# Kernel optimization log

Hardware: AMD Instinct MI355X
Metric: run time of the kernel (lower is better)

Reference implementation:

```python
import jax, jax.numpy as jnp
import numpy as np


def layer_norm(x, gamma, beta, eps=1e-6):
    # Torch module uses unbiased std (ddof=1) and divides by (std + eps)
    mean = x.mean(-1, keepdims=True)
    std = jnp.std(x, axis=-1, keepdims=True, ddof=1)
    return gamma * (x - mean) / (std + eps) + beta


def gelu_erf(x):
    return 0.5 * x * (1.0 + jax.lax.erf(x / jnp.sqrt(jnp.asarray(2.0, x.dtype))))


def setup_inputs() -> dict:
    B, S, D, H, F = 32, 512, 1024, 16, 4096
    key = jax.random.key(0)
    ks = jax.random.split(key, 16)
    w = lambda k, shp: (jax.random.normal(k, shp, jnp.float32) * 0.02)
    return {
        "x": jax.random.normal(ks[0], (B, S, D), jnp.float32),
        "mask": jax.random.randint(ks[1], (B, S), 0, 2).astype(jnp.int32),
        "adj": jax.random.normal(ks[2], (B, 1, S, S), jnp.float32) * 0.1,
        "num_head": H,
        "Wq": w(ks[3], (D, D)), "bq": jnp.zeros((D,), jnp.float32),
        "Wk": w(ks[4], (D, D)), "bk": jnp.zeros((D,), jnp.float32),
        "Wv": w(ks[5], (D, D)), "bv": jnp.zeros((D,), jnp.float32),
        "Wo": w(ks[6], (D, D)), "bo": jnp.zeros((D,), jnp.float32),
        "W1": w(ks[7], (D, F)), "b1": jnp.zeros((F,), jnp.float32),
        "W2": w(ks[8], (F, D)), "b2": jnp.zeros((D,), jnp.float32),
        "gamma": jnp.ones((D,), jnp.float32),
        "beta": jnp.zeros((D,), jnp.float32),
    }


def reference(x, mask, adj, num_head, Wq, bq, Wk, bk, Wv, bv, Wo, bo,
              W1, b1, W2, b2, gamma, beta):
    B, S, D = x.shape
    H = num_head
    dk = D // H
    split = lambda t: t.reshape(B, S, H, dk).transpose(0, 2, 1, 3)  # [B,H,S,dk]
    q = split(x @ Wq + bq)
    k = split(x @ Wk + bk)
    v = split(x @ Wv + bv)
    scores = jnp.einsum('bhqd,bhkd->bhqk', q, k) / np.float32(np.sqrt(dk))
    m = mask[:, None, None, :].astype(x.dtype)  # [B,1,1,S]
    scores = scores + m * jnp.asarray(-1e9, x.dtype) + adj
    attn = jax.nn.softmax(scores, axis=-1)
    ctx = jnp.einsum('bhqk,bhkd->bhqd', attn, v)
    ctx = ctx.transpose(0, 2, 1, 3).reshape(B, S, D)
    attn_out = ctx @ Wo + bo  # dropout is identity at eval
    out1 = layer_norm(x + attn_out, gamma, beta)
    ffn = gelu_erf(out1 @ W1 + b1) @ W2 + b2
    return layer_norm(out1 + ffn, gamma, beta)
```

## Files before the change

### kernel.cpp

```cpp
#include <hip/hip_runtime.h>
#include <stdint.h>
#include <math.h>

typedef unsigned short u16;
typedef __attribute__((ext_vector_type(8))) __bf16 bf16x8;
typedef __attribute__((ext_vector_type(4))) float f32x4;
typedef __attribute__((ext_vector_type(4))) unsigned short u16x4;

__device__ __forceinline__ float b2f(u16 u) {
    unsigned int i = ((unsigned int)u) << 16;
    float f; __builtin_memcpy(&f, &i, 4); return f;
}
__device__ __forceinline__ u16 f2b(float f) {
    unsigned int i; __builtin_memcpy(&i, &f, 4);
    i = (i + 0x7FFFu + ((i >> 16) & 1u)) >> 16;
    return (u16)i;
}
__device__ __forceinline__ bf16x8 ld8_cvt(const float* p) {
    float4 f0 = *(const float4*)p, f1 = *(const float4*)(p + 4);
    u16 t[8] = {f2b(f0.x), f2b(f0.y), f2b(f0.z), f2b(f0.w),
                f2b(f1.x), f2b(f1.y), f2b(f1.z), f2b(f1.w)};
    bf16x8 r; __builtin_memcpy(&r, t, 16); return r;
}

__device__ __forceinline__ void glds16(const u16* g, u16* l) {
    __builtin_amdgcn_global_load_lds(
        (const __attribute__((address_space(1))) void*)g,
        (__attribute__((address_space(3))) void*)l, 16, 0, 0);
}

__global__ __launch_bounds__(256) void transpose_f32_bf16(
    const float* __restrict__ in, u16* __restrict__ out, int R, int C)
{
    __shared__ float t[32][33];
    int bx = blockIdx.x * 32, by = blockIdx.y * 32;
    int x = threadIdx.x, y = threadIdx.y;
    #pragma unroll
    for (int j = 0; j < 32; j += 8)
        t[y + j][x] = in[(size_t)(by + y + j) * C + bx + x];
    __syncthreads();
    #pragma unroll
    for (int j = 0; j < 32; j += 8)
        out[(size_t)(bx + y + j) * R + by + x] = f2b(t[x][y + j]);
}

__global__ __launch_bounds__(256) void cvt_f32_bf16(
    const float* __restrict__ in, u16* __restrict__ out)
{
    size_t i = ((size_t)blockIdx.x * 256 + threadIdx.x) * 8;
    *(bf16x8*)(out + i) = ld8_cvt(in + i);
}

template<int EPI, int BN>
__global__ __launch_bounds__(256) void gemm_bt(
    const u16* __restrict__ A, const u16* __restrict__ Bt, int N, int K,
    u16* __restrict__ C, const float* __restrict__ bias,
    u16* __restrict__ qo, u16* __restrict__ ko, u16* __restrict__ vo,
    const float* __restrict__ bq, const float* __restrict__ bk,
    const float* __restrict__ bv)
{
    __shared__ __align__(16) u16 Asm[128 * 32];
    __shared__ __align__(16) u16 Bsm[BN * 32];
    const int tid  = threadIdx.x;
    const int lane = tid & 63;
    const int wave = tid >> 6;
    const int lrow = lane & 15, quad = lane >> 4;
    const int bm = blockIdx.x * 128, bn = blockIdx.y * BN;

    const int srow = tid >> 2;
    const int skol = (tid & 3) * 8;
    const u16* gA0 = A  + (size_t)(bm + srow) * K + skol;
    const u16* gA1 = gA0 + (size_t)64 * K;
    const u16* gB0 = Bt + (size_t)(bn + srow) * K + skol;
    const u16* gB1 = gB0 + (size_t)64 * K;

    const int wm = wave >> 1, wn = wave & 1;
    const int NT = (BN == 128) ? 4 : 2;
    f32x4 acc[4][(BN == 128) ? 4 : 2] = {};

    for (int kt = 0; kt < K; kt += 32) {
        __syncthreads();
        glds16(gA0 + kt, &Asm[(size_t)tid * 8]);
        glds16(gA1 + kt, &Asm[((size_t)tid + 256) * 8]);
        glds16(gB0 + kt, &Bsm[(size_t)tid * 8]);
        if (BN == 128) glds16(gB1 + kt, &Bsm[((size_t)tid + 256) * 8]);
        __syncthreads();

        bf16x8 af[4], bfr[(BN == 128) ? 4 : 2];
        #pragma unroll
        for (int mt = 0; mt < 4; mt++)
            af[mt] = *(const bf16x8*)&Asm[(wm * 64 + mt * 16 + lrow) * 32 + quad * 8];
        #pragma unroll
        for (int nt = 0; nt < NT; nt++)
            bfr[nt] = *(const bf16x8*)&Bsm[(wn * (BN / 2) + nt * 16 + lrow) * 32 + quad * 8];
        #pragma unroll
        for (int mt = 0; mt < 4; mt++)
            #pragma unroll
            for (int nt = 0; nt < NT; nt++)
                acc[mt][nt] = __builtin_amdgcn_mfma_f32_16x16x32_bf16(
                    af[mt], bfr[nt], acc[mt][nt], 0, 0, 0);
    }

    #pragma unroll
    for (int nt = 0; nt < NT; nt++) {
        int col = bn + wn * (BN / 2) + nt * 16 + lrow;
        int mat = 0, hh = 0, dd = 0;
        float bval;
        if (EPI == 2) {
            mat  = col >> 10; int dcol = col & 1023;
            hh = dcol >> 6;   dd = dcol & 63;
            const float* bp = (mat == 0) ? bq : ((mat == 1) ? bk : bv);
            bval = bp[dcol];
        } else {
            bval = bias[col];
        }
        #pragma unroll
        for (int mt = 0; mt < 4; mt++) {
            #pragma unroll
            for (int r = 0; r < 4; r++) {
                int row = bm + wm * 64 + mt * 16 + quad * 4 + r;
                float v = acc[mt][nt][r] + bval;
                if (EPI == 1) v = 0.5f * v * (1.0f + erff(v * 0.70710678118654752f));
                if (EPI == 2) {
                    int b = row >> 9, s = row & 511;
                    u16* dst = (mat == 0) ? qo : ((mat == 1) ? ko : vo);
                    dst[(((size_t)(b * 16 + hh)) * 512 + s) * 64 + dd] = f2b(v);
                } else {
                    C[(size_t)row * N + col] = f2b(v);
                }
            }
        }
    }
}

__global__ __launch_bounds__(256) void attn_kernel(
    const u16* __restrict__ Q, const u16* __restrict__ Kb, const u16* __restrict__ Vb,
    const float* __restrict__ adj, const int* __restrict__ mask, u16* __restrict__ ctx)
{
    const int S = 512, H = 16;
    __shared__ __align__(16) u16 Ksm[32 * 64];
    __shared__ __align__(16) u16 Vt [64 * 32];
    __shared__ __align__(16) u16 Psm[4][16 * 32];

    int tid = threadIdx.x, lane = tid & 63, wave = tid >> 6;
    int lrow = lane & 15, quad = lane >> 4;
    int qt = blockIdx.x, h = blockIdx.y, b = blockIdx.z;

    size_t headoff = ((size_t)(b * H + h)) * S * 64;
    const u16* qp = Q + headoff;
    const u16* kp = Kb + headoff;
    const u16* vp = Vb + headoff;
    const float* adjb = adj + (size_t)b * S * S;
    const int* maskb = mask + b * S;
    int q0 = qt * 64 + wave * 16;

    bf16x8 qf0 = *(const bf16x8*)(qp + (size_t)(q0 + lrow) * 64 + quad * 8);
    bf16x8 qf1 = *(const bf16x8*)(qp + (size_t)(q0 + lrow) * 64 + 32 + quad * 8);

    float m_run[4] = {-1e30f, -1e30f, -1e30f, -1e30f};
    float l_run[4] = {0.f, 0.f, 0.f, 0.f};
    f32x4 o[4] = {};

    int str = tid >> 3;
    int stc = (tid & 7) * 8;

    for (int kt = 0; kt < S; kt += 32) {
        __syncthreads();
        glds16(kp + (size_t)(kt + str) * 64 + stc, &Ksm[str * 64 + stc]);
        {
            bf16x8 vv = *(const bf16x8*)(vp + (size_t)(kt + str) * 64 + stc);
            const u16* tv = (const u16*)&vv;
            #pragma unroll
            for (int j = 0; j < 8; j++) Vt[(stc + j) * 32 + str] = tv[j];
        }
        __syncthreads();

        f32x4 sc[2];
        #pragma unroll
        for (int f = 0; f < 2; f++) {
            f32x4 cf = {};
            bf16x8 kf0 = *(const bf16x8*)&Ksm[(f * 16 + lrow) * 64 + quad * 8];
            bf16x8 kf1 = *(const bf16x8*)&Ksm[(f * 16 + lrow) * 64 + 32 + quad * 8];
            cf = __builtin_amdgcn_mfma_f32_16x16x32_bf16(qf0, kf0, cf, 0, 0, 0);
            cf = __builtin_amdgcn_mfma_f32_16x16x32_bf16(qf1, kf1, cf, 0, 0, 0);
            int key = kt + f * 16 + lrow;
            float mterm = maskb[key] ? -1e9f : 0.0f;
            #pragma unroll
            for (int r = 0; r < 4; r++) {
                int qrow = q0 + quad * 4 + r;
                sc[f][r] = cf[r] * 0.125f + mterm + adjb[(size_t)qrow * S + key];
            }
        }

        float mx[4], al[4], sm[4];
        #pragma unroll
        for (int r = 0; r < 4; r++) mx[r] = fmaxf(sc[0][r], sc[1][r]);
        #pragma unroll
        for (int mk = 1; mk < 16; mk <<= 1)
            #pragma unroll
            for (int r = 0; r < 4; r++) mx[r] = fmaxf(mx[r], __shfl_xor(mx[r], mk));
        #pragma unroll
        for (int r = 0; r < 4; r++) {
            float mn = fmaxf(m_run[r], mx[r]);
            al[r] = __expf(fminf(m_run[r] - mn, 0.f));
            m_run[r] = mn;
        }
        #pragma unroll
        for (int f = 0; f < 2; f++)
            #pragma unroll
            for (int r = 0; r < 4; r++)
                sc[f][r] = __expf(fminf(sc[f][r] - m_run[r], 0.f));
        #pragma unroll
        for (int r = 0; r < 4; r++) sm[r] = sc[0][r] + sc[1][r];
        #pragma unroll
        for (int mk = 1; mk < 16; mk <<= 1)
            #pragma unroll
            for (int r = 0; r < 4; r++) sm[r] += __shfl_xor(sm[r], mk);
        #pragma unroll
        for (int r = 0; r < 4; r++) l_run[r] = l_run[r] * al[r] + sm[r];
        #pragma unroll
        for (int nt = 0; nt < 4; nt++)
            #pragma unroll
            for (int r = 0; r < 4; r++) o[nt][r] *= al[r];

        #pragma unroll
        for (int f = 0; f < 2; f++)
            #pragma unroll
            for (int r = 0; r < 4; r++)
                Psm[wave][(quad * 4 + r) * 32 + f * 16 + lrow] = f2b(sc[f][r]);
        bf16x8 pa = *(const bf16x8*)&Psm[wave][lrow * 32 + quad * 8];
        #pragma unroll
        for (int nt = 0; nt < 4; nt++) {
            bf16x8 vf = *(const bf16x8*)&Vt[(nt * 16 + lrow) * 32 + quad * 8];
            o[nt] = __builtin_amdgcn_mfma_f32_16x16x32_bf16(pa, vf, o[nt], 0, 0, 0);
        }
    }

    #pragma unroll
    for (int nt = 0; nt < 4; nt++)
        #pragma unroll
        for (int r = 0; r < 4; r++) {
            int qrow = q0 + quad * 4 + r;
            ctx[((size_t)b * 512 + qrow) * 1024 + h * 64 + nt * 16 + lrow] =
                f2b(o[nt][r] / l_run[r]);
        }
}

template<int MODE>
__global__ __launch_bounds__(256) void add_ln(
    const void* __restrict__ Xv, const void* __restrict__ Yv,
    const float* __restrict__ gamma, const float* __restrict__ beta,
    void* __restrict__ outv)
{
    const int D = 1024;
    int row = blockIdx.x, tid = threadIdx.x;
    int lane = tid & 63, wave = tid >> 6;
    size_t base = (size_t)row * D + tid * 4;

    float x[4];
    if (MODE == 0) {
        float4 xf = *(const float4*)((const float*)Xv + base);
        u16x4  uy = *(const u16x4*)((const u16*)Yv + base);
        x[0] = xf.x + b2f(uy[0]); x[1] = xf.y + b2f(uy[1]);
        x[2] = xf.z + b2f(uy[2]); x[3] = xf.w + b2f(uy[3]);
    } else {
        u16x4 ux = *(const u16x4*)((const u16*)Xv + base);
        u16x4 uy = *(const u16x4*)((const u16*)Yv + base);
        #pragma unroll
        for (int j = 0; j < 4; j++) x[j] = b2f(ux[j]) + b2f(uy[j]);
    }

    float s = x[0] + x[1] + x[2] + x[3];
    #pragma unroll
    for (int mk = 1; mk < 64; mk <<= 1) s += __shfl_xor(s, mk);
    __shared__ float red[8];
    if (lane == 0) red[wave] = s;
    __syncthreads();
    float mean = (red[0] + red[1] + red[2] + red[3]) * (1.0f / 1024.0f);

    float c[4], q = 0.f;
    #pragma unroll
    for (int j = 0; j < 4; j++) { c[j] = x[j] - mean; q += c[j] * c[j]; }
    #pragma unroll
    for (int mk = 1; mk < 64; mk <<= 1) q += __shfl_xor(q, mk);
    if (lane == 0) red[4 + wave] = q;
    __syncthreads();
    float var = (red[4] + red[5] + red[6] + red[7]) * (1.0f / 1023.0f);
    float inv = 1.0f / (sqrtf(var) + 1e-6f);

    float4 g4 = *(const float4*)(gamma + tid * 4);
    float4 b4 = *(const float4*)(beta + tid * 4);
    float gv[4] = {g4.x, g4.y, g4.z, g4.w};
    float bv[4] = {b4.x, b4.y, b4.z, b4.w};
    if (MODE == 0) {
        u16x4 ov;
        #pragma unroll
        for (int j = 0; j < 4; j++) ov[j] = f2b(gv[j] * c[j] * inv + bv[j]);
        *(u16x4*)((u16*)outv + base) = ov;
    } else {
        float4 ov;
        ov.x = gv[0] * c[0] * inv + bv[0];
        ov.y = gv[1] * c[1] * inv + bv[1];
        ov.z = gv[2] * c[2] * inv + bv[2];
        ov.w = gv[3] * c[3] * inv + bv[3];
        *(float4*)((float*)outv + base) = ov;
    }
}

extern "C" void kernel_launch(void* const* d_in, const int* in_sizes, int n_in,
                              void* d_out, int out_size, void* d_ws, size_t ws_size,
                              hipStream_t stream)
{
    const float* x    = (const float*)d_in[0];
    const int*   mask = (const int*)d_in[1];
    const float* adj  = (const float*)d_in[2];
    const float* Wq = (const float*)d_in[4];  const float* bq = (const float*)d_in[5];
    const float* Wk = (const float*)d_in[6];  const float* bk = (const float*)d_in[7];
    const float* Wv = (const float*)d_in[8];  const float* bv = (const float*)d_in[9];
    const float* Wo = (const float*)d_in[10]; const float* bo = (const float*)d_in[11];
    const float* W1 = (const float*)d_in[12]; const float* b1 = (const float*)d_in[13];
    const float* W2 = (const float*)d_in[14]; const float* b2 = (const float*)d_in[15];
    const float* gamma = (const float*)d_in[16];
    const float* beta  = (const float*)d_in[17];
    float* out = (float*)d_out;

    const size_t MB = 1024ull * 1024;
    char* w = (char*)d_ws;
    u16* Wqkv_t = (u16*)(w + 0 * MB);
    u16* Wo_t   = (u16*)(w + 6 * MB);
    u16* W1_t   = (u16*)(w + 8 * MB);
    u16* W2_t   = (u16*)(w + 16 * MB);
    u16* out1   = (u16*)(w + 24 * MB);
    u16* qg     = (u16*)(w + 56 * MB);
    u16* kg     = (u16*)(w + 64 * MB);
    u16* vg     = (u16*)(w + 72 * MB);
    u16* ctxg   = (u16*)(w + 80 * MB);
    u16* aog    = (u16*)(w + 88 * MB);
    u16* hid    = (u16*)(w + 56 * MB);
    u16* ffn    = (u16*)(w + 88 * MB);

    dim3 tb(32, 8);
    transpose_f32_bf16<<<dim3(32, 32),  tb, 0, stream>>>(Wq, Wqkv_t,                1024, 1024);
    transpose_f32_bf16<<<dim3(32, 32),  tb, 0, stream>>>(Wk, Wqkv_t + 1024ull*1024, 1024, 1024);
    transpose_f32_bf16<<<dim3(32, 32),  tb, 0, stream>>>(Wv, Wqkv_t + 2048ull*1024, 1024, 1024);
    transpose_f32_bf16<<<dim3(32, 32),  tb, 0, stream>>>(Wo, Wo_t,                  1024, 1024);
    transpose_f32_bf16<<<dim3(128, 32), tb, 0, stream>>>(W1, W1_t,                  1024, 4096);
    transpose_f32_bf16<<<dim3(32, 128), tb, 0, stream>>>(W2, W2_t,                  4096, 1024);

    for (int g = 0; g < 4; g++) {
        const float* xg = x + (size_t)g * 4096 * 1024;
        cvt_f32_bf16<<<2048, 256, 0, stream>>>(xg, aog);
        gemm_bt<2, 128><<<dim3(32, 24), 256, 0, stream>>>(aog, Wqkv_t, 3072, 1024,
            nullptr, nullptr, qg, kg, vg, bq, bk, bv);
        attn_kernel<<<dim3(8, 16, 8), 256, 0, stream>>>(qg, kg, vg,
            adj + (size_t)g * 8 * 512 * 512, mask + g * 8 * 512, ctxg);
        gemm_bt<0, 64><<<dim3(32, 16), 256, 0, stream>>>(ctxg, Wo_t, 1024, 1024,
            aog, bo, nullptr, nullptr, nullptr, nullptr, nullptr, nullptr);
        add_ln<0><<<4096, 256, 0, stream>>>(xg, aog, gamma, beta,
            out1 + (size_t)g * 4096 * 1024);
    }

    for (int c = 0; c < 4; c++) {
        const u16* o1c = out1 + (size_t)c * 4096 * 1024;
        gemm_bt<1, 128><<<dim3(32, 32), 256, 0, stream>>>(o1c, W1_t, 4096, 1024,
            hid, b1, nullptr, nullptr, nullptr, nullptr, nullptr, nullptr);
        gemm_bt<0, 64><<<dim3(32, 16), 256, 0, stream>>>(hid, W2_t, 1024, 4096,
            ffn, b2, nullptr, nullptr, nullptr, nullptr, nullptr, nullptr);
        add_ln<1><<<4096, 256, 0, stream>>>(o1c, ffn, gamma, beta,
            out + (size_t)c * 4096 * 1024);
    }
}
```

Baseline: 1.321 ms.

## Double-buffer LDS tiles in GEMM and attention, and remap block order

The GEMM and attention kernels now keep two LDS buffers, so the next K-tile is fetched while the current one feeds the MFMAs, and each loop iteration needs one barrier instead of two. The attention kernel also loads its adj values ahead of the score computation so their latency overlaps the QK MFMAs. Both kernels permute the flat block index so that consecutive blocks land on different groups, with the goal of better cache locality across the device. The cost is twice the LDS, which may lower occupancy, and the GEMM remap assumes the block count is divisible by eight.

```diff
diff --git a/kernel.cpp b/kernel.cpp
--- a/kernel.cpp
+++ b/kernel.cpp
@@ -59,13 +59,18 @@
     const float* __restrict__ bq, const float* __restrict__ bk,
     const float* __restrict__ bv)
 {
-    __shared__ __align__(16) u16 Asm[128 * 32];
-    __shared__ __align__(16) u16 Bsm[BN * 32];
+    __shared__ __align__(16) u16 Asm[2][128 * 32];
+    __shared__ __align__(16) u16 Bsm[2][BN * 32];
     const int tid  = threadIdx.x;
     const int lane = tid & 63;
     const int wave = tid >> 6;
     const int lrow = lane & 15, quad = lane >> 4;
-    const int bm = blockIdx.x * 128, bn = blockIdx.y * BN;
+
+    const int gx = gridDim.x;
+    const int nwg = gx * gridDim.y;
+    const int orig = blockIdx.y * gx + blockIdx.x;
+    const int wg = (orig & 7) * (nwg >> 3) + (orig >> 3);
+    const int bm = (wg % gx) * 128, bn = (wg / gx) * BN;
 
     const int srow = tid >> 2;
     const int skol = (tid & 3) * 8;
@@ -75,30 +80,41 @@
     const u16* gB1 = gB0 + (size_t)64 * K;
 
     const int wm = wave >> 1, wn = wave & 1;
-    const int NT = (BN == 128) ? 4 : 2;
-    f32x4 acc[4][(BN == 128) ? 4 : 2] = {};
-
+    constexpr int NT = (BN == 128) ? 4 : 2;
+    f32x4 acc[4][NT] = {};
+
+    glds16(gA0, &Asm[0][(size_t)tid * 8]);
+    glds16(gA1, &Asm[0][((size_t)tid + 256) * 8]);
+    glds16(gB0, &Bsm[0][(size_t)tid * 8]);
+    if (BN == 128) glds16(gB1, &Bsm[0][((size_t)tid + 256) * 8]);
+    __syncthreads();
+
+    int cur = 0;
     for (int kt = 0; kt < K; kt += 32) {
-        __syncthreads();
-        glds16(gA0 + kt, &Asm[(size_t)tid * 8]);
-        glds16(gA1 + kt, &Asm[((size_t)tid + 256) * 8]);
-        glds16(gB0 + kt, &Bsm[(size_t)tid * 8]);
-        if (BN == 128) glds16(gB1 + kt, &Bsm[((size_t)tid + 256) * 8]);
-        __syncthreads();
-
-        bf16x8 af[4], bfr[(BN == 128) ? 4 : 2];
+        const int nxt = kt + 32;
+        if (nxt < K) {
+            glds16(gA0 + nxt, &Asm[cur ^ 1][(size_t)tid * 8]);
+            glds16(gA1 + nxt, &Asm[cur ^ 1][((size_t)tid + 256) * 8]);
+            glds16(gB0 + nxt, &Bsm[cur ^ 1][(size_t)tid * 8]);
+            if (BN == 128) glds16(gB1 + nxt, &Bsm[cur ^ 1][((size_t)tid + 256) * 8]);
+        }
+
+        bf16x8 af[4], bfr[NT];
         #pragma unroll
         for (int mt = 0; mt < 4; mt++)
-            af[mt] = *(const bf16x8*)&Asm[(wm * 64 + mt * 16 + lrow) * 32 + quad * 8];
+            af[mt] = *(const bf16x8*)&Asm[cur][(wm * 64 + mt * 16 + lrow) * 32 + quad * 8];
         #pragma unroll
         for (int nt = 0; nt < NT; nt++)
-            bfr[nt] = *(const bf16x8*)&Bsm[(wn * (BN / 2) + nt * 16 + lrow) * 32 + quad * 8];
+            bfr[nt] = *(const bf16x8*)&Bsm[cur][(wn * (BN / 2) + nt * 16 + lrow) * 32 + quad * 8];
         #pragma unroll
         for (int mt = 0; mt < 4; mt++)
             #pragma unroll
             for (int nt = 0; nt < NT; nt++)
                 acc[mt][nt] = __builtin_amdgcn_mfma_f32_16x16x32_bf16(
                     af[mt], bfr[nt], acc[mt][nt], 0, 0, 0);
+
+        __syncthreads();
+        cur ^= 1;
     }
 
     #pragma unroll
@@ -138,13 +154,17 @@
     const float* __restrict__ adj, const int* __restrict__ mask, u16* __restrict__ ctx)
 {
     const int S = 512, H = 16;
-    __shared__ __align__(16) u16 Ksm[32 * 64];
-    __shared__ __align__(16) u16 Vt [64 * 32];
+    __shared__ __align__(16) u16 Ksm[2][32 * 64];
+    __shared__ __align__(16) u16 Vt [2][64 * 32];
     __shared__ __align__(16) u16 Psm[4][16 * 32];
 
     int tid = threadIdx.x, lane = tid & 63, wave = tid >> 6;
     int lrow = lane & 15, quad = lane >> 4;
-    int qt = blockIdx.x, h = blockIdx.y, b = blockIdx.z;
+
+    int orig = (blockIdx.z * 16 + blockIdx.y) * 8 + blockIdx.x;
+    int b  = orig & 7;
+    int h  = (orig >> 3) & 15;
+    int qt = orig >> 7;
 
     size_t headoff = ((size_t)(b * H + h)) * S * 64;
     const u16* qp = Q + headoff;
@@ -164,32 +184,43 @@
     int str = tid >> 3;
     int stc = (tid & 7) * 8;
 
+    glds16(kp + (size_t)str * 64 + stc, &Ksm[0][str * 64 + stc]);
+    bf16x8 vcur = *(const bf16x8*)(vp + (size_t)str * 64 + stc);
+    __syncthreads();
+
+    int cur = 0;
     for (int kt = 0; kt < S; kt += 32) {
-        __syncthreads();
-        glds16(kp + (size_t)(kt + str) * 64 + stc, &Ksm[str * 64 + stc]);
+        const int nxt = kt + 32;
+        bf16x8 vnxt;
+        if (nxt < S) {
+            glds16(kp + (size_t)(nxt + str) * 64 + stc, &Ksm[cur ^ 1][str * 64 + stc]);
+            vnxt = *(const bf16x8*)(vp + (size_t)(nxt + str) * 64 + stc);
+        }
         {
-            bf16x8 vv = *(const bf16x8*)(vp + (size_t)(kt + str) * 64 + stc);
-            const u16* tv = (const u16*)&vv;
-            #pragma unroll
-            for (int j = 0; j < 8; j++) Vt[(stc + j) * 32 + str] = tv[j];
-        }
-        __syncthreads();
+            const u16* tv = (const u16*)&vcur;
+            #pragma unroll
+            for (int j = 0; j < 8; j++) Vt[cur][(stc + j) * 32 + str] = tv[j];
+        }
+        float adjv[2][4];
+        #pragma unroll
+        for (int f = 0; f < 2; f++)
+            #pragma unroll
+            for (int r = 0; r < 4; r++)
+                adjv[f][r] = adjb[(size_t)(q0 + quad * 4 + r) * S + kt + f * 16 + lrow];
 
         f32x4 sc[2];
         #pragma unroll
         for (int f = 0; f < 2; f++) {
             f32x4 cf = {};
-            bf16x8 kf0 = *(const bf16x8*)&Ksm[(f * 16 + lrow) * 64 + quad * 8];
-            bf16x8 kf1 = *(const bf16x8*)&Ksm[(f * 16 + lrow) * 64 + 32 + quad * 8];
+            bf16x8 kf0 = *(const bf16x8*)&Ksm[cur][(f * 16 + lrow) * 64 + quad * 8];
+            bf16x8 kf1 = *(const bf16x8*)&Ksm[cur][(f * 16 + lrow) * 64 + 32 + quad * 8];
             cf = __builtin_amdgcn_mfma_f32_16x16x32_bf16(qf0, kf0, cf, 0, 0, 0);
             cf = __builtin_amdgcn_mfma_f32_16x16x32_bf16(qf1, kf1, cf, 0, 0, 0);
             int key = kt + f * 16 + lrow;
             float mterm = maskb[key] ? -1e9f : 0.0f;
             #pragma unroll
-            for (int r = 0; r < 4; r++) {
-                int qrow = q0 + quad * 4 + r;
-                sc[f][r] = cf[r] * 0.125f + mterm + adjb[(size_t)qrow * S + key];
-            }
+            for (int r = 0; r < 4; r++)
+                sc[f][r] = cf[r] * 0.125f + mterm + adjv[f][r];
         }
 
         float mx[4], al[4], sm[4];
@@ -229,11 +260,15 @@
             for (int r = 0; r < 4; r++)
                 Psm[wave][(quad * 4 + r) * 32 + f * 16 + lrow] = f2b(sc[f][r]);
         bf16x8 pa = *(const bf16x8*)&Psm[wave][lrow * 32 + quad * 8];
+
+        __syncthreads();
         #pragma unroll
         for (int nt = 0; nt < 4; nt++) {
-            bf16x8 vf = *(const bf16x8*)&Vt[(nt * 16 + lrow) * 32 + quad * 8];
+            bf16x8 vf = *(const bf16x8*)&Vt[cur][(nt * 16 + lrow) * 32 + quad * 8];
             o[nt] = __builtin_amdgcn_mfma_f32_16x16x32_bf16(pa, vf, o[nt], 0, 0, 0);
         }
+        if (nxt < S) vcur = vnxt;
+        cur ^= 1;
     }
 
     #pragma unroll
```

After: 1.274 ms. -3.6%, faster.
